# Optimization experiments

Measured on AMD Instinct MI355X. Metric: run time of the kernel, lower is better.

Reference implementation:

```python
import jax, jax.numpy as jnp
import numpy as np

NEG_INF = -1e10  # matches torch masked_fill value -10000000000.0


def setup_inputs() -> dict:
    key = jax.random.key(0)
    k1, k2, k3, k4 = jax.random.split(key, 4)
    B, Lq, Lk, D = 8, 2048, 2048, 1024
    hidden = jax.random.normal(k1, (B, Lq, D), dtype=jnp.float32)
    keys = jax.random.normal(k2, (B, Lk, D), dtype=jnp.float32)
    values = jax.random.normal(k3, (B, Lk, D), dtype=jnp.float32)
    mask = jax.random.randint(k4, (B, Lk), 0, 2, dtype=jnp.int32)
    return {"hidden": hidden, "keys": keys, "values": values, "mask": mask}


def reference(hidden, keys, values, mask):
    # scores[b,q,k] = sum_d hidden[b,q,d] * keys[b,k,d]  (unscaled dot-product)
    scores = jnp.einsum("bqd,bkd->bqk", hidden, keys)
    scores = jnp.where(mask[:, None, :] == 0, NEG_INF, scores)
    weights = jax.nn.softmax(scores, axis=2)  # (B, Lq, Lk)
    # context[b,q,d] = sum_k weights[b,q,k] * values[b,k,d]
    context = jnp.einsum("bqk,bkd->bqd", weights, values)
    return context
```

## Files before the change

### kernel.cpp

```cpp
#include <hip/hip_runtime.h>

#define NEG_INF -1e10f
#define B_   8
#define LQ_  2048
#define LK_  2048
#define D_   1024

typedef unsigned int uint;
typedef unsigned short u16;
typedef _Float16 f16;
typedef _Float16 f16x8_t __attribute__((ext_vector_type(8)));
typedef float f32x4_t __attribute__((ext_vector_type(4)));

__device__ __forceinline__ u16 f2h_bits(float f) {
    f16 h = (f16)f;
    return __builtin_bit_cast(u16, h);
}
__device__ __forceinline__ void gload_lds16(const void* g, void* l) {
    __builtin_amdgcn_global_load_lds(
        (const __attribute__((address_space(1))) uint*)g,
        (__attribute__((address_space(3))) uint*)l, 16, 0, 0);
}

__global__ __launch_bounds__(256) void convert_f16_2(
    const float4* __restrict__ s1, ushort4* __restrict__ d1,
    const float4* __restrict__ s2, ushort4* __restrict__ d2, int n4)
{
    int idx = blockIdx.x * 256 + threadIdx.x;
    const int stride = gridDim.x * 256;
    for (; idx < 2 * n4; idx += stride) {
        const bool second = idx >= n4;
        const int i = second ? idx - n4 : idx;
        float4 x = second ? s2[i] : s1[i];
        ushort4 h;
        h.x = f2h_bits(x.x);
        h.y = f2h_bits(x.y);
        h.z = f2h_bits(x.z);
        h.w = f2h_bits(x.w);
        if (second) d2[i] = h; else d1[i] = h;
    }
}

__global__ __launch_bounds__(256) void transpose_convert(
    const float* __restrict__ V, u16* __restrict__ VT)
{
    __shared__ float tile[64][65];
    const int t  = threadIdx.x;
    const int d0 = blockIdx.x * 64;
    const int k0 = blockIdx.y * 64;
    const float* Vb = V + (size_t)blockIdx.z * (LK_ * D_);
    u16* VTb = VT + (size_t)blockIdx.z * (D_ * LK_);
#pragma unroll
    for (int i = 0; i < 4; ++i) {
        int f = i * 256 + t;
        int r = f >> 4, c4 = f & 15;
        float4 v = *(const float4*)&Vb[(size_t)(k0 + r) * D_ + d0 + c4 * 4];
        tile[r][c4 * 4 + 0] = v.x;
        tile[r][c4 * 4 + 1] = v.y;
        tile[r][c4 * 4 + 2] = v.z;
        tile[r][c4 * 4 + 3] = v.w;
    }
    __syncthreads();
#pragma unroll
    for (int i = 0; i < 4; ++i) {
        int f = i * 256 + t;
        int d = f >> 4, c4 = f & 15;
        ushort4 o;
        o.x = f2h_bits(tile[c4 * 4 + 0][d]);
        o.y = f2h_bits(tile[c4 * 4 + 1][d]);
        o.z = f2h_bits(tile[c4 * 4 + 2][d]);
        o.w = f2h_bits(tile[c4 * 4 + 3][d]);
        *(ushort4*)&VTb[(size_t)(d0 + d) * LK_ + k0 + c4 * 4] = o;
    }
}

#define BM_  256
#define BK_  32

template<int NBF, int NTILES, bool SPLIT>
__global__ __launch_bounds__(512, 2) void gemm8p(
    const u16* __restrict__ A0g, const u16* __restrict__ A1g,
    const u16* __restrict__ Bg, float* __restrict__ Cg,
    int lda, int ldb, int ldc, int bkmask,
    size_t szA, size_t szB, size_t szC)
{
    constexpr int BN     = 64 * NBF;
    constexpr int ABYTES = BM_ * BK_ * 2;
    constexpr int BBYTES = BN * BK_ * 2;
    constexpr int BUFSZ  = ABYTES + BBYTES;
    __shared__ char lds[4 * BUFSZ];

    const int tid  = threadIdx.x;
    const int lane = tid & 63;
    const int w    = tid >> 6;
    const int wm   = w >> 2;
    const int wn   = w & 3;

    const int d  = blockIdx.x;
    const int g  = d & 7;
    const int k_ = d >> 3;
    int by, bx;
    if constexpr (!SPLIT) {
        by = (g >> 1) * 2 + (k_ & 1);
        bx = (g & 1) * 4 + (k_ >> 1);
    } else {
        by = (g >> 1) * 2 + (k_ & 1);
        bx = (g & 1) * 2 + (k_ >> 1);
    }
    const int m0 = by * BM_;
    const int n0 = bx * BN;
    const size_t z = blockIdx.y;

    const u16* A0 = A0g + z * szA;
    const u16* A1 = A1g + z * szA;
    const u16* B  = Bg  + z * szB;
    float* C = Cg + z * szC;

    const int  lr   = lane & 15;
    const uint csel = (uint)((((lane >> 4) ^ ((lane >> 1) & 3)) * 16));
    const int  cstg = (((lane & 3) ^ ((lane >> 3) & 3)) * 8);
    const int  rstg = lane >> 2;

    const uint awoff = (uint)(wm * 8192 + lr * 64) + csel;
    const uint bwoff = (uint)(wn * (NBF * 1024) + lr * 64) + csel;

    f32x4_t acc[8][NBF];
#pragma unroll
    for (int m = 0; m < 8; ++m)
#pragma unroll
        for (int n = 0; n < NBF; ++n)
            acc[m][n] = (f32x4_t){0.f, 0.f, 0.f, 0.f};

    auto stA = [&](int t) {
        const u16* Ab;
        int kc;
        if constexpr (SPLIT) {
            Ab = (t < NTILES / 2) ? A0 : A1;
            kc = (t & (NTILES / 2 - 1)) * BK_ + cstg;
        } else {
            Ab = A0;
            kc = t * BK_ + cstg;
        }
        char* dst = lds + (t & 3) * BUFSZ + w * 2048;
        gload_lds16(&Ab[(size_t)(m0 + w * 32 + rstg) * lda + kc], dst);
        gload_lds16(&Ab[(size_t)(m0 + w * 32 + 16 + rstg) * lda + kc], dst + 1024);
    };
    auto stB = [&](int t) {
        const int kc = ((t * BK_) & bkmask) + cstg;
        char* dst = lds + (t & 3) * BUFSZ + ABYTES;
        gload_lds16(&B[(size_t)(n0 + w * 32 + rstg) * ldb + kc], dst + w * 2048);
        gload_lds16(&B[(size_t)(n0 + w * 32 + 16 + rstg) * ldb + kc], dst + w * 2048 + 1024);
    };

    stA(0); stB(0); stA(1); stB(1); stA(2); stB(2);
    asm volatile("s_waitcnt vmcnt(8)" ::: "memory");
    __builtin_amdgcn_s_barrier();

#define LDF(p) (*(const f16x8_t*)(p))

#define PHASE_A(T, DOSTAGE)                                                   \
    {                                                                         \
        const char* pA = lds + ((T) & 3) * BUFSZ + awoff;                     \
        const char* pB = lds + ((T) & 3) * BUFSZ + ABYTES + bwoff;            \
        f16x8_t a[4], b[NBF];                                                 \
        a[0] = LDF(pA);        a[1] = LDF(pA + 1024);                         \
        a[2] = LDF(pA + 2048); a[3] = LDF(pA + 3072);                         \
        b[0] = LDF(pB);        b[1] = LDF(pB + 1024);                         \
        b[2] = LDF(pB + 2048); b[3] = LDF(pB + 3072);                         \
        if (DOSTAGE) stA((T) + 3);                                            \
        __builtin_amdgcn_s_barrier();                                         \
        __builtin_amdgcn_s_setprio(1);                                        \
        _Pragma("unroll")                                                     \
        for (int mf = 0; mf < 4; ++mf)                                        \
            _Pragma("unroll")                                                 \
            for (int nf = 0; nf < NBF; ++nf)                                  \
                acc[mf][nf] = __builtin_amdgcn_mfma_f32_16x16x32_f16(         \
                    a[mf], b[nf], acc[mf][nf], 0, 0, 0);                      \
        __builtin_amdgcn_s_setprio(0);                                        \
        bsave[0] = b[0]; bsave[1] = b[1]; bsave[2] = b[2]; bsave[3] = b[3];   \
        __builtin_amdgcn_s_barrier();                                         \
    }

#define PHASE_B(T, DOSTAGE, VMASM)                                            \
    {                                                                         \
        const char* pA = lds + ((T) & 3) * BUFSZ + awoff;                     \
        f16x8_t a[4];                                                         \
        a[0] = LDF(pA + 4096); a[1] = LDF(pA + 5120);                         \
        a[2] = LDF(pA + 6144); a[3] = LDF(pA + 7168);                         \
        if (DOSTAGE) stB((T) + 3);                                            \
        __builtin_amdgcn_s_barrier();                                         \
        __builtin_amdgcn_s_setprio(1);                                        \
        _Pragma("unroll")                                                     \
        for (int mf = 0; mf < 4; ++mf)                                        \
            _Pragma("unroll")                                                 \
            for (int nf = 0; nf < NBF; ++nf)                                  \
                acc[4 + mf][nf] = __builtin_amdgcn_mfma_f32_16x16x32_f16(     \
                    a[mf], bsave[nf], acc[4 + mf][nf], 0, 0, 0);              \
        __builtin_amdgcn_s_setprio(0);                                        \
        VMASM;                                                                \
        __builtin_amdgcn_s_barrier();                                         \
    }

#define VMW asm volatile("s_waitcnt vmcnt(8)" ::: "memory")
#define VMH asm volatile("s_waitcnt vmcnt(4)" ::: "memory")
#define VM0 asm volatile("s_waitcnt vmcnt(0)" ::: "memory")
#define VMN do {} while (0)

    f16x8_t bsave[NBF];

    for (int t = 0; t < NTILES - 3; ++t) {
        PHASE_A(t, true);
        PHASE_B(t, true, VMW);
    }
    PHASE_A(NTILES - 3, false); PHASE_B(NTILES - 3, false, VMH);
    PHASE_A(NTILES - 2, false); PHASE_B(NTILES - 2, false, VM0);
    PHASE_A(NTILES - 1, false); PHASE_B(NTILES - 1, false, VMN);
#undef PHASE_A
#undef PHASE_B
#undef LDF

    const int cg = lane >> 4;
#pragma unroll
    for (int mf = 0; mf < 8; ++mf)
#pragma unroll
        for (int nf = 0; nf < NBF; ++nf) {
            const int row = m0 + wm * 128 + mf * 16 + cg * 4;
            const int col = n0 + wn * (NBF * 16) + nf * 16 + lr;
#pragma unroll
            for (int r = 0; r < 4; ++r)
                C[(size_t)(row + r) * ldc + col] = acc[mf][nf][r];
        }
}

__global__ __launch_bounds__(256) void softmax_mask(
    float* __restrict__ S, const int* __restrict__ mask0)
{
    const int lane = threadIdx.x & 63;
    const int wave = threadIdx.x >> 6;
    const int row  = blockIdx.x * 4 + wave;
    const size_t zb = blockIdx.y;
    float* Sr = S + (zb * LQ_ + row) * (size_t)LK_;
    const int* mb = mask0 + zb * LK_;

    float4 s[8];
    float m = -INFINITY;
#pragma unroll
    for (int i = 0; i < 8; ++i) {
        int k = i * 256 + lane * 4;
        float4 v = *(const float4*)&Sr[k];
        int4 mk  = *(const int4*)&mb[k];
        v.x = mk.x ? v.x : NEG_INF;
        v.y = mk.y ? v.y : NEG_INF;
        v.z = mk.z ? v.z : NEG_INF;
        v.w = mk.w ? v.w : NEG_INF;
        s[i] = v;
        m = fmaxf(m, fmaxf(fmaxf(v.x, v.y), fmaxf(v.z, v.w)));
    }
#pragma unroll
    for (int off = 32; off > 0; off >>= 1)
        m = fmaxf(m, __shfl_xor(m, off, 64));
    float sum = 0.f;
#pragma unroll
    for (int i = 0; i < 8; ++i) {
        s[i].x = __expf(s[i].x - m); sum += s[i].x;
        s[i].y = __expf(s[i].y - m); sum += s[i].y;
        s[i].z = __expf(s[i].z - m); sum += s[i].z;
        s[i].w = __expf(s[i].w - m); sum += s[i].w;
    }
#pragma unroll
    for (int off = 32; off > 0; off >>= 1)
        sum += __shfl_xor(sum, off, 64);
    const float inv = 1.f / sum;
    u16* Pr = (u16*)Sr;
#pragma unroll
    for (int i = 0; i < 8; ++i) {
        int k = i * 256 + lane * 4;
        ushort4 o;
        o.x = f2h_bits(s[i].x * inv);
        o.y = f2h_bits(s[i].y * inv);
        o.z = f2h_bits(s[i].z * inv);
        o.w = f2h_bits(s[i].w * inv);
        *(ushort4*)&Pr[k] = o;
    }
}

__global__ __launch_bounds__(256, 2) void attn_fp32_flash(
    const float* __restrict__ hidden, const float* __restrict__ keys,
    const float* __restrict__ values, const int* __restrict__ mask,
    float* __restrict__ out)
{
    const int lane = threadIdx.x & 63;
    const int wave = threadIdx.x >> 6;
    const int blk  = blockIdx.x;
    const int b    = blk >> 7;
    const int q0   = (blk & 127) * 16 + wave * 4;
    float4 q[4][4]; float4 o[4][4]; float m[4], s[4];
    const float4* hp = (const float4*)(hidden + ((size_t)b * LQ_ + q0) * D_);
#pragma unroll
    for (int r = 0; r < 4; ++r) {
#pragma unroll
        for (int j = 0; j < 4; ++j) {
            q[r][j] = hp[r * 256 + j * 64 + lane];
            o[r][j] = make_float4(0.f, 0.f, 0.f, 0.f);
        }
        m[r] = -INFINITY; s[r] = 0.f;
    }
    const float4* kp = (const float4*)(keys   + (size_t)b * LK_ * D_);
    const float4* vp = (const float4*)(values + (size_t)b * LK_ * D_);
    const int*    mp = mask + b * LK_;
    for (int k = 0; k < LK_; ++k) {
        float4 kv[4];
#pragma unroll
        for (int j = 0; j < 4; ++j) kv[j] = kp[k * 256 + j * 64 + lane];
        float sc[4];
#pragma unroll
        for (int r = 0; r < 4; ++r) {
            float p = 0.f;
#pragma unroll
            for (int j = 0; j < 4; ++j)
                p += q[r][j].x * kv[j].x + q[r][j].y * kv[j].y +
                     q[r][j].z * kv[j].z + q[r][j].w * kv[j].w;
            sc[r] = p;
        }
#pragma unroll
        for (int r = 0; r < 4; ++r)
#pragma unroll
            for (int off = 32; off > 0; off >>= 1)
                sc[r] += __shfl_xor(sc[r], off, 64);
        const int mk = mp[k];
        float4 vv[4];
#pragma unroll
        for (int j = 0; j < 4; ++j) vv[j] = vp[k * 256 + j * 64 + lane];
#pragma unroll
        for (int r = 0; r < 4; ++r) {
            float score = mk ? sc[r] : NEG_INF;
            if (score > m[r]) {
                float scale = __expf(m[r] - score);
                m[r] = score; s[r] *= scale;
#pragma unroll
                for (int j = 0; j < 4; ++j) {
                    o[r][j].x *= scale; o[r][j].y *= scale;
                    o[r][j].z *= scale; o[r][j].w *= scale;
                }
            }
            float e = __expf(score - m[r]);
            s[r] += e;
#pragma unroll
            for (int j = 0; j < 4; ++j) {
                o[r][j].x += e * vv[j].x; o[r][j].y += e * vv[j].y;
                o[r][j].z += e * vv[j].z; o[r][j].w += e * vv[j].w;
            }
        }
    }
    float4* op = (float4*)(out + ((size_t)b * LQ_ + q0) * D_);
#pragma unroll
    for (int r = 0; r < 4; ++r) {
        float inv = 1.f / s[r];
#pragma unroll
        for (int j = 0; j < 4; ++j) {
            float4 t = o[r][j];
            t.x *= inv; t.y *= inv; t.z *= inv; t.w *= inv;
            op[r * 256 + j * 64 + lane] = t;
        }
    }
}

extern "C" void kernel_launch(void* const* d_in, const int* in_sizes, int n_in,
                              void* d_out, int out_size, void* d_ws, size_t ws_size,
                              hipStream_t stream) {
    const float* hidden = (const float*)d_in[0];
    const float* keys   = (const float*)d_in[1];
    const float* values = (const float*)d_in[2];
    const int*   mask   = (const int*)d_in[3];
    float* out = (float*)d_out;
    char* ws = (char*)d_ws;

    const size_t TEN = (size_t)LK_ * D_;
    const size_t MB  = 1024ull * 1024;

    int BG = 0;
    for (int g = 8; g >= 1; g >>= 1)
        if ((size_t)g * 28 * MB <= ws_size) { BG = g; break; }

    if (BG == 0) {
        attn_fp32_flash<<<1024, 256, 0, stream>>>(hidden, keys, values, mask, out);
        return;
    }

    const size_t SZ_BF = (size_t)BG * TEN * 2;
    u16*   Kh = (u16*)(ws);
    u16*   VT = (u16*)(ws + SZ_BF);
    u16*   Qh = (u16*)(ws + 2 * SZ_BF);
    float* S  = (float*)(ws + 3 * SZ_BF);

    const int n4 = BG * (int)(TEN / 4);

    for (int bg0 = 0; bg0 < B_; bg0 += BG) {
        const size_t off = (size_t)bg0 * TEN;
        convert_f16_2<<<4096, 256, 0, stream>>>(
            (const float4*)(keys + off), (ushort4*)Kh,
            (const float4*)(hidden + off), (ushort4*)Qh, n4);
        transpose_convert<<<dim3(16, 32, BG), 256, 0, stream>>>(
            values + off, VT);

        gemm8p<4, 32, false><<<dim3(64, BG), 512, 0, stream>>>(
            Qh, Qh, Kh, S, D_, D_, LK_, 1023,
            TEN, TEN, (size_t)LQ_ * LK_);

        softmax_mask<<<dim3(LQ_ / 4, BG), 256, 0, stream>>>(
            S, mask + bg0 * LK_);

        gemm8p<4, 64, true><<<dim3(32, BG), 512, 0, stream>>>(
            (const u16*)S, (const u16*)S + 1024, VT, out + off,
            2 * LK_, LK_, D_, 2047,
            (size_t)LQ_ * 2 * LK_, TEN, (size_t)LQ_ * D_);
    }
}
```

Before: 238.9 us.

## Add dedicated double-buffered QK GEMM kernel with inline-asm LDS reads

Replaces the templated 4-stage gemm8p for the QK^T score GEMM with a new gemm_qk2 kernel. It uses a 2-buffer LDS pipeline with one barrier per k-tile and issues ds_read_b128 through inline asm with immediate offsets. It also splits the MFMA work into two halves gated by partial lgkmcnt waits and raises wave priority during compute. The shallower prefetch (vmcnt(0) each iteration) may expose more global-load latency in exchange for fewer address calculations and less LDS use. gemm8p is simplified to the split-A PV variant only.

Result: no change. 236.3 us, median of 2 (-1.1%).

```diff
diff --git a/kernel.cpp b/kernel.cpp
--- a/kernel.cpp
+++ b/kernel.cpp
@@ -74,16 +74,120 @@
     }
 }
 
+#define DSR(dst, base, off) \
+    asm volatile("ds_read_b128 %0, %1 offset:" off : "=v"(dst) : "v"(base))
+
+__global__ __launch_bounds__(512, 2) void gemm_qk2(
+    const u16* __restrict__ Ag, const u16* __restrict__ Bg,
+    float* __restrict__ Cg, size_t szA, size_t szB, size_t szC)
+{
+    constexpr int NT     = 32;
+    constexpr int ABYTES = 256 * 32 * 2;
+    constexpr int BUFSZ  = 2 * ABYTES;
+    __shared__ char lds[2 * BUFSZ];
+
+    const int tid  = threadIdx.x;
+    const int lane = tid & 63;
+    const int w    = tid >> 6;
+    const int wm   = w >> 2;
+    const int wn   = w & 3;
+
+    const int d  = blockIdx.x;
+    const int g  = d & 7;
+    const int k_ = d >> 3;
+    const int m0 = ((g >> 1) * 2 + (k_ & 1)) * 256;
+    const int n0 = ((g & 1) * 4 + (k_ >> 1)) * 256;
+    const size_t z = blockIdx.y;
+
+    const u16* A = Ag + z * szA;
+    const u16* B = Bg + z * szB;
+    float* C = Cg + z * szC;
+
+    const uint ldsbase = (uint)(size_t)&lds[0];
+    const int  lr   = lane & 15;
+    const uint csel = (uint)((((lane >> 4) ^ ((lane >> 1) & 3)) * 16));
+    const int  cstg = (((lane & 3) ^ ((lane >> 3) & 3)) * 8);
+    const int  rstg = lane >> 2;
+
+    const uint awoff = (uint)(wm * 8192 + lr * 64) + csel;
+    const uint bwoff = (uint)(wn * 4096 + lr * 64) + csel;
+
+    f32x4_t acc[8][4];
+#pragma unroll
+    for (int m = 0; m < 8; ++m)
+#pragma unroll
+        for (int n = 0; n < 4; ++n)
+            acc[m][n] = (f32x4_t){0.f, 0.f, 0.f, 0.f};
+
+    auto stage = [&](int t) {
+        const int kc = t * 32 + cstg;
+        char* dA = lds + (t & 1) * BUFSZ + w * 2048;
+        char* dB = lds + (t & 1) * BUFSZ + ABYTES + w * 2048;
+        gload_lds16(&A[(size_t)(m0 + w * 32 + rstg) * D_ + kc], dA);
+        gload_lds16(&A[(size_t)(m0 + w * 32 + 16 + rstg) * D_ + kc], dA + 1024);
+        gload_lds16(&B[(size_t)(n0 + w * 32 + rstg) * D_ + kc], dB);
+        gload_lds16(&B[(size_t)(n0 + w * 32 + 16 + rstg) * D_ + kc], dB + 1024);
+    };
+
+    stage(0);
+
+    f16x8_t a0[4], a1[4], b[4];
+    for (int t = 0; t < NT; ++t) {
+        asm volatile("s_waitcnt vmcnt(0)" ::: "memory");
+        __builtin_amdgcn_s_barrier();
+        if (t + 1 < NT) stage(t + 1);
+        const uint aA = ldsbase + (uint)((t & 1) * BUFSZ) + awoff;
+        const uint aB = ldsbase + (uint)((t & 1) * BUFSZ + ABYTES) + bwoff;
+        DSR(b[0], aB, "0");     DSR(b[1], aB, "1024");
+        DSR(b[2], aB, "2048");  DSR(b[3], aB, "3072");
+        DSR(a0[0], aA, "0");    DSR(a0[1], aA, "1024");
+        DSR(a0[2], aA, "2048"); DSR(a0[3], aA, "3072");
+        DSR(a1[0], aA, "4096"); DSR(a1[1], aA, "5120");
+        DSR(a1[2], aA, "6144"); DSR(a1[3], aA, "7168");
+        asm volatile("s_waitcnt lgkmcnt(4)");
+        __builtin_amdgcn_sched_barrier(0);
+        __builtin_amdgcn_s_setprio(1);
+#pragma unroll
+        for (int mf = 0; mf < 4; ++mf)
+#pragma unroll
+            for (int nf = 0; nf < 4; ++nf)
+                acc[mf][nf] = __builtin_amdgcn_mfma_f32_16x16x32_f16(
+                    a0[mf], b[nf], acc[mf][nf], 0, 0, 0);
+        asm volatile("s_waitcnt lgkmcnt(0)");
+        __builtin_amdgcn_sched_barrier(0);
+#pragma unroll
+        for (int mf = 0; mf < 4; ++mf)
+#pragma unroll
+            for (int nf = 0; nf < 4; ++nf)
+                acc[4 + mf][nf] = __builtin_amdgcn_mfma_f32_16x16x32_f16(
+                    a1[mf], b[nf], acc[4 + mf][nf], 0, 0, 0);
+        __builtin_amdgcn_s_setprio(0);
+    }
+
+    const int cg = lane >> 4;
+#pragma unroll
+    for (int mf = 0; mf < 8; ++mf)
+#pragma unroll
+        for (int nf = 0; nf < 4; ++nf) {
+            const int row = m0 + wm * 128 + mf * 16 + cg * 4;
+            const int col = n0 + wn * 64 + nf * 16 + lr;
+#pragma unroll
+            for (int r = 0; r < 4; ++r)
+                C[(size_t)(row + r) * LK_ + col] = acc[mf][nf][r];
+        }
+}
+
 #define BM_  256
 #define BK_  32
 
-template<int NBF, int NTILES, bool SPLIT>
+template<int NTILES>
 __global__ __launch_bounds__(512, 2) void gemm8p(
     const u16* __restrict__ A0g, const u16* __restrict__ A1g,
     const u16* __restrict__ Bg, float* __restrict__ Cg,
     int lda, int ldb, int ldc, int bkmask,
     size_t szA, size_t szB, size_t szC)
 {
+    constexpr int NBF    = 4;
     constexpr int BN     = 64 * NBF;
     constexpr int ABYTES = BM_ * BK_ * 2;
     constexpr int BBYTES = BN * BK_ * 2;
@@ -99,14 +203,8 @@
     const int d  = blockIdx.x;
     const int g  = d & 7;
     const int k_ = d >> 3;
-    int by, bx;
-    if constexpr (!SPLIT) {
-        by = (g >> 1) * 2 + (k_ & 1);
-        bx = (g & 1) * 4 + (k_ >> 1);
-    } else {
-        by = (g >> 1) * 2 + (k_ & 1);
-        bx = (g & 1) * 2 + (k_ >> 1);
-    }
+    const int by = (g >> 1) * 2 + (k_ & 1);
+    const int bx = (g & 1) * 2 + (k_ >> 1);
     const int m0 = by * BM_;
     const int n0 = bx * BN;
     const size_t z = blockIdx.y;
@@ -132,15 +230,8 @@
             acc[m][n] = (f32x4_t){0.f, 0.f, 0.f, 0.f};
 
     auto stA = [&](int t) {
-        const u16* Ab;
-        int kc;
-        if constexpr (SPLIT) {
-            Ab = (t < NTILES / 2) ? A0 : A1;
-            kc = (t & (NTILES / 2 - 1)) * BK_ + cstg;
-        } else {
-            Ab = A0;
-            kc = t * BK_ + cstg;
-        }
+        const u16* Ab = (t < NTILES / 2) ? A0 : A1;
+        const int kc = (t & (NTILES / 2 - 1)) * BK_ + cstg;
         char* dst = lds + (t & 3) * BUFSZ + w * 2048;
         gload_lds16(&Ab[(size_t)(m0 + w * 32 + rstg) * lda + kc], dst);
         gload_lds16(&Ab[(size_t)(m0 + w * 32 + 16 + rstg) * lda + kc], dst + 1024);
@@ -403,14 +494,13 @@
         transpose_convert<<<dim3(16, 32, BG), 256, 0, stream>>>(
             values + off, VT);
 
-        gemm8p<4, 32, false><<<dim3(64, BG), 512, 0, stream>>>(
-            Qh, Qh, Kh, S, D_, D_, LK_, 1023,
-            TEN, TEN, (size_t)LQ_ * LK_);
+        gemm_qk2<<<dim3(64, BG), 512, 0, stream>>>(
+            Qh, Kh, S, TEN, TEN, (size_t)LQ_ * LK_);
 
         softmax_mask<<<dim3(LQ_ / 4, BG), 256, 0, stream>>>(
             S, mask + bg0 * LK_);
 
-        gemm8p<4, 64, true><<<dim3(32, BG), 512, 0, stream>>>(
+        gemm8p<64><<<dim3(32, BG), 512, 0, stream>>>(
             (const u16*)S, (const u16*)S + 1024, VT, out + off,
             2 * LK_, LK_, D_, 2047,
             (size_t)LQ_ * 2 * LK_, TEN, (size_t)LQ_ * D_);
```

## Have each QK^T block compute two stacked row tiles with a mid-loop store

Applied to the files above, without the earlier changes.

The QK^T GEMM now launches half as many blocks. Each block processes two 256-row tiles of Q back to back in one 64-step K loop, reusing the B-side (K matrix) tile column. The accumulators for the first tile are written out and zeroed halfway through, so the prologue and epilogue are paid once per two tiles and the pipeline stays full. The cost is a mid-loop store stall and fewer blocks, which can leave the GPU less full.

Result: no change. 237.5 us (-0.6%).

```diff
diff --git a/kernel.cpp b/kernel.cpp
--- a/kernel.cpp
+++ b/kernel.cpp
@@ -77,13 +77,14 @@
 #define BM_  256
 #define BK_  32
 
-template<int NBF, int NTILES, bool SPLIT>
+template<int NTILES, bool MIDC>
 __global__ __launch_bounds__(512, 2) void gemm8p(
     const u16* __restrict__ A0g, const u16* __restrict__ A1g,
     const u16* __restrict__ Bg, float* __restrict__ Cg,
     int lda, int ldb, int ldc, int bkmask,
     size_t szA, size_t szB, size_t szC)
 {
+    constexpr int NBF    = 4;
     constexpr int BN     = 64 * NBF;
     constexpr int ABYTES = BM_ * BK_ * 2;
     constexpr int BBYTES = BN * BK_ * 2;
@@ -99,16 +100,18 @@
     const int d  = blockIdx.x;
     const int g  = d & 7;
     const int k_ = d >> 3;
-    int by, bx;
-    if constexpr (!SPLIT) {
-        by = (g >> 1) * 2 + (k_ & 1);
-        bx = (g & 1) * 4 + (k_ >> 1);
+    int m0, n0;
+    if constexpr (MIDC) {
+        const int j = g >> 1;
+        const int n = (g & 1) * 4 + k_;
+        m0 = j * 512;
+        n0 = n * 256;
     } else {
-        by = (g >> 1) * 2 + (k_ & 1);
-        bx = (g & 1) * 2 + (k_ >> 1);
-    }
-    const int m0 = by * BM_;
-    const int n0 = bx * BN;
+        const int by = (g >> 1) * 2 + (k_ & 1);
+        const int bx = (g & 1) * 2 + (k_ >> 1);
+        m0 = by * 256;
+        n0 = bx * 256;
+    }
     const size_t z = blockIdx.y;
 
     const u16* A0 = A0g + z * szA;
@@ -132,15 +135,8 @@
             acc[m][n] = (f32x4_t){0.f, 0.f, 0.f, 0.f};
 
     auto stA = [&](int t) {
-        const u16* Ab;
-        int kc;
-        if constexpr (SPLIT) {
-            Ab = (t < NTILES / 2) ? A0 : A1;
-            kc = (t & (NTILES / 2 - 1)) * BK_ + cstg;
-        } else {
-            Ab = A0;
-            kc = t * BK_ + cstg;
-        }
+        const u16* Ab = (t < NTILES / 2) ? A0 : A1;
+        const int kc = (t & (NTILES / 2 - 1)) * BK_ + cstg;
         char* dst = lds + (t & 3) * BUFSZ + w * 2048;
         gload_lds16(&Ab[(size_t)(m0 + w * 32 + rstg) * lda + kc], dst);
         gload_lds16(&Ab[(size_t)(m0 + w * 32 + 16 + rstg) * lda + kc], dst + 1024);
@@ -150,6 +146,20 @@
         char* dst = lds + (t & 3) * BUFSZ + ABYTES;
         gload_lds16(&B[(size_t)(n0 + w * 32 + rstg) * ldb + kc], dst + w * 2048);
         gload_lds16(&B[(size_t)(n0 + w * 32 + 16 + rstg) * ldb + kc], dst + w * 2048 + 1024);
+    };
+
+    const int cg = lane >> 4;
+    auto writeC = [&](int rowbase) {
+#pragma unroll
+        for (int mf = 0; mf < 8; ++mf)
+#pragma unroll
+            for (int nf = 0; nf < NBF; ++nf) {
+                const int row = rowbase + wm * 128 + mf * 16 + cg * 4;
+                const int col = n0 + wn * (NBF * 16) + nf * 16 + lr;
+#pragma unroll
+                for (int r = 0; r < 4; ++r)
+                    C[(size_t)(row + r) * ldc + col] = acc[mf][nf][r];
+            }
     };
 
     stA(0); stB(0); stA(1); stB(1); stA(2); stB(2);
@@ -211,6 +221,16 @@
     for (int t = 0; t < NTILES - 3; ++t) {
         PHASE_A(t, true);
         PHASE_B(t, true, VMW);
+        if constexpr (MIDC) {
+            if (t == NTILES / 2 - 1) {
+                writeC(m0);
+#pragma unroll
+                for (int m = 0; m < 8; ++m)
+#pragma unroll
+                    for (int n = 0; n < NBF; ++n)
+                        acc[m][n] = (f32x4_t){0.f, 0.f, 0.f, 0.f};
+            }
+        }
     }
     PHASE_A(NTILES - 3, false); PHASE_B(NTILES - 3, false, VMH);
     PHASE_A(NTILES - 2, false); PHASE_B(NTILES - 2, false, VM0);
@@ -219,17 +239,7 @@
 #undef PHASE_B
 #undef LDF
 
-    const int cg = lane >> 4;
-#pragma unroll
-    for (int mf = 0; mf < 8; ++mf)
-#pragma unroll
-        for (int nf = 0; nf < NBF; ++nf) {
-            const int row = m0 + wm * 128 + mf * 16 + cg * 4;
-            const int col = n0 + wn * (NBF * 16) + nf * 16 + lr;
-#pragma unroll
-            for (int r = 0; r < 4; ++r)
-                C[(size_t)(row + r) * ldc + col] = acc[mf][nf][r];
-        }
+    writeC(m0 + (MIDC ? 256 : 0));
 }
 
 __global__ __launch_bounds__(256) void softmax_mask(
@@ -403,14 +413,14 @@
         transpose_convert<<<dim3(16, 32, BG), 256, 0, stream>>>(
             values + off, VT);
 
-        gemm8p<4, 32, false><<<dim3(64, BG), 512, 0, stream>>>(
-            Qh, Qh, Kh, S, D_, D_, LK_, 1023,
+        gemm8p<64, true><<<dim3(32, BG), 512, 0, stream>>>(
+            Qh, Qh + 256 * D_, Kh, S, D_, D_, LK_, 1023,
             TEN, TEN, (size_t)LQ_ * LK_);
 
         softmax_mask<<<dim3(LQ_ / 4, BG), 256, 0, stream>>>(
             S, mask + bg0 * LK_);
 
-        gemm8p<4, 64, true><<<dim3(32, BG), 512, 0, stream>>>(
+        gemm8p<64, false><<<dim3(32, BG), 512, 0, stream>>>(
             (const u16*)S, (const u16*)S + 1024, VT, out + off,
             2 * LK_, LK_, D_, 2047,
             (size_t)LQ_ * 2 * LK_, TEN, (size_t)LQ_ * D_);
```
